# Optimization experiments

Measured on AMD Instinct MI355X. Metric: run time of the kernel, lower is better.

Reference implementation:

```python
import jax, jax.numpy as jnp
import numpy as np

B, T, L, A, O = 16, 32, 64, 64, 16
EL, EA, EO = 128, 128, 128
FL, FA, FO, C = 256, 256, 256, 768


def setup_inputs() -> dict:
    key = jax.random.key(0)
    ks = jax.random.split(key, 16)
    s = 0.02
    return {
        "lab_feats": jax.random.normal(ks[0], (B, T, L, FL), jnp.float32),
        "abn_feats": jax.random.normal(ks[1], (B, T, A, FA), jnp.float32),
        "lab_concept_emb": jax.random.normal(ks[2], (L, C), jnp.float32),
        "abn_concept_emb": jax.random.normal(ks[3], (A, C), jnp.float32),
        "lab_rel_emb": jax.random.normal(ks[4], (EL, C), jnp.float32),
        "abn_rel_emb": jax.random.normal(ks[5], (EA, C), jnp.float32),
        "W_lab": jax.random.normal(ks[6], (FL + C, FL), jnp.float32) * s,
        "b_lab": jnp.zeros((FL,), jnp.float32),
        "W_abn": jax.random.normal(ks[7], (FA + C, FA), jnp.float32) * s,
        "b_abn": jnp.zeros((FA,), jnp.float32),
        "W_org": jax.random.normal(ks[8], (FL, FO), jnp.float32) * s,
        "b_org": jnp.zeros((FO,), jnp.float32),
        "D": jax.random.normal(ks[9], (C, FL), jnp.float32) * s,
        "W_o2a": jax.random.normal(ks[10], (FO, FA), jnp.float32) * s,
        "b_o2a": jnp.zeros((FA,), jnp.float32),
        "time_mask": jnp.ones((B, T), dtype=bool),
        "lab_idx": jax.random.randint(ks[11], (EL,), 0, L),
        "lab_org_idx": jax.random.randint(ks[12], (EL,), 0, O),
        "abn_idx": jax.random.randint(ks[13], (EA,), 0, A),
        "abn_org_idx": jax.random.randint(ks[14], (EA,), 0, O),
        "o2a_abn_idx": jax.random.randint(ks[15], (EO,), 0, A),
        "o2a_org_idx": jax.random.randint(jax.random.fold_in(key, 99), (EO,), 0, O),
        "num_organs": O,
    }


def _scatter_mean(attended, org_idx, num_organs, time_mask):
    # attended: (B,T,E,F); emulate legacy per-edge accumulate: cnt[o] = deg(o)*w(b,t)
    onehot = (org_idx[:, None] == jnp.arange(num_organs)[None, :]).astype(attended.dtype)  # (E,O)
    sum_o = jnp.einsum('btef,eo->btof', attended, onehot)
    deg = onehot.sum(0)                                    # (O,)
    w = time_mask.astype(attended.dtype)                   # (B,T)
    cnt = w[:, :, None] * deg[None, None, :]               # (B,T,O)
    mean_o = sum_o / jnp.maximum(cnt, 1e-9)[..., None]
    return mean_o, cnt > 0


def reference(lab_feats, abn_feats, lab_concept_emb, abn_concept_emb,
              lab_rel_emb, abn_rel_emb, W_lab, b_lab, W_abn, b_abn,
              W_org, b_org, D, W_o2a, b_o2a,
              time_mask, lab_idx, lab_org_idx, abn_idx, abn_org_idx,
              o2a_abn_idx, o2a_org_idx, num_organs):
    Fl = lab_feats.shape[-1]
    Fa = abn_feats.shape[-1]
    A_ = abn_feats.shape[2]

    # --- lab -> organ: gather, concat(feat, concept+relation), W_lab (split to avoid concat) ---
    x = lab_feats[:, :, lab_idx, :]                        # (B,T,El,Fl)
    c = lab_concept_emb[lab_idx] + lab_rel_emb             # (El,C)
    h = jnp.tanh(jnp.einsum('btef,fg->bteg', x, W_lab[:Fl]) + c @ W_lab[Fl:] + b_lab)
    attended = h + lab_rel_emb @ D                         # relation-projection D
    mean_lab, mask_lab = _scatter_mean(attended, lab_org_idx, num_organs, time_mask)

    # --- abn -> organ ---
    xa = abn_feats[:, :, abn_idx, :]
    ca = abn_concept_emb[abn_idx] + abn_rel_emb
    ha = jnp.tanh(jnp.einsum('btef,fg->bteg', xa, W_abn[:Fa]) + ca @ W_abn[Fa:] + b_abn)
    mean_abn, mask_abn = _scatter_mean(ha, abn_org_idx, num_organs, time_mask)

    # --- organ states ---
    organ_states = jnp.tanh(jnp.einsum('btof,fg->btog', mean_lab + mean_abn, W_org) + b_org)
    organ_states = organ_states * (mask_lab | mask_abn)[..., None].astype(organ_states.dtype)

    # --- organ -> abnormality message passing (mean over incident organs) ---
    msg = jnp.einsum('btog,gf->btof', organ_states, W_o2a) + b_o2a   # (B,T,O,Fa)
    gathered = msg[:, :, o2a_org_idx, :]                   # (B,T,Eo,Fa)
    onehot = (o2a_abn_idx[:, None] == jnp.arange(A_)[None, :]).astype(msg.dtype)  # (Eo,A)
    agg = jnp.einsum('btef,ea->btaf', gathered, onehot)
    deg = jnp.maximum(onehot.sum(0), 1.0)                  # (A,)
    abn_out = abn_feats + agg / deg[None, None, :, None]
    return abn_out
```

## Files before the change

### kernel.cpp

```cpp
#include <hip/hip_runtime.h>
#include <math.h>

#define NBT 512
#define NF  256
#define NC  768
#define NROW 64
#define NORG 16
#define NE  128
#define SLD 260
#define SY  264
#define SSR 776

#define WS_SW_LAB1 0
#define WS_SW_ABN1 131072
#define WS_SW_ORG  1441792
#define WS_SW_O2A  1572864
#define WS_LAB_CB  1753088
#define WS_ABN_CB  1884160
#define WS_ADDSUM  2015232
#define WS_WCNT    2031616
#define WS_INVL    2035712
#define WS_INVA    2035776
#define WS_MASK    2035840
#define WS_SRTL    2035904
#define WS_SRTA    2036544
#define WS_NEED    2097152

typedef __attribute__((ext_vector_type(8)))  short bf16x8;
typedef __attribute__((ext_vector_type(16))) float f32x16;
typedef __attribute__((ext_vector_type(4)))  float f32x4;

__device__ __forceinline__ short f2bf(float f) {
    union { float f; unsigned u; } v; v.f = f;
    unsigned r = v.u + 0x7FFF + ((v.u >> 16) & 1);
    return (short)(r >> 16);
}
__device__ __forceinline__ float bf2f(short s) {
    return __uint_as_float(((unsigned)(unsigned short)s) << 16);
}
__device__ __forceinline__ float tanh_fast(float x) {
    float xc = fminf(fmaxf(x, -15.f), 15.f);
    float e = __expf(2.f * xc);
    return 1.f - 2.f * __builtin_amdgcn_rcpf(e + 1.f);
}
__device__ __forceinline__ f32x16 mfma32(bf16x8 a, bf16x8 b, f32x16 c) {
    return __builtin_amdgcn_mfma_f32_32x32x16_bf16(a, b, c, 0, 0, 0);
}
__device__ __forceinline__ f32x4 mfma16(bf16x8 a, bf16x8 b, f32x4 c) {
    return __builtin_amdgcn_mfma_f32_16x16x32_bf16(a, b, c, 0, 0, 0);
}
__device__ __forceinline__ bf16x8 pack_a16(const float* __restrict__ p) {
    float4 x0 = *(const float4*)p;
    float4 x1 = *(const float4*)(p + 4);
    union { bf16x8 v; unsigned u[4]; } r;
    r.u[0] = __builtin_amdgcn_perm(__float_as_uint(x0.y), __float_as_uint(x0.x), 0x07060302);
    r.u[1] = __builtin_amdgcn_perm(__float_as_uint(x0.w), __float_as_uint(x0.z), 0x07060302);
    r.u[2] = __builtin_amdgcn_perm(__float_as_uint(x1.y), __float_as_uint(x1.x), 0x07060302);
    r.u[3] = __builtin_amdgcn_perm(__float_as_uint(x1.w), __float_as_uint(x1.z), 0x07060302);
    return r.v;
}

__device__ __forceinline__ void swz32(const float* __restrict__ src, short* __restrict__ dst, int s) {
    const int l = s & 63, rest = s >> 6;
    const int nt = rest & 7, k16 = rest >> 3;
    const int n = nt * 32 + (l & 31);
    const int kb = k16 * 16 + ((l >> 5) & 1) * 8;
    bf16x8 v;
    #pragma unroll
    for (int j = 0; j < 8; ++j) v[j] = f2bf(src[(kb + j) * NF + n]);
    *(bf16x8*)(dst + s * 8) = v;
}
__device__ __forceinline__ void swz16(const float* __restrict__ src, short* __restrict__ dst, int s) {
    const int l = s & 63, rest = s >> 6;
    const int nt = rest & 15, k32 = rest >> 4;
    const int n = nt * 16 + (l & 15);
    const int kb = k32 * 32 + ((l >> 4) & 3) * 8;
    bf16x8 v;
    #pragma unroll
    for (int j = 0; j < 8; ++j) v[j] = f2bf(src[(kb + j) * NF + n]);
    *(bf16x8*)(dst + s * 8) = v;
}

__global__ __launch_bounds__(256) void pk_pre2(
    const float* __restrict__ W_lab, const float* __restrict__ W_abn,
    const float* __restrict__ W_org,
    const float* __restrict__ W_o2a, const float* __restrict__ D,
    const float* __restrict__ lab_rel,
    const float* __restrict__ lab_con, const float* __restrict__ abn_con,
    const float* __restrict__ abn_rel,
    const float* __restrict__ b_lab, const float* __restrict__ b_abn,
    const int* __restrict__ lab_idx, const int* __restrict__ lab_org_idx,
    const int* __restrict__ abn_idx, const int* __restrict__ abn_org_idx,
    const int* __restrict__ o2a_abn_idx, const int* __restrict__ o2a_org_idx,
    char* __restrict__ ws) {
    __shared__ __align__(16) float sP[4 * 1024];
    __shared__ __align__(16) short sSR[NORG * SSR];
    const int bid = blockIdx.x;
    const int tid = threadIdx.x;
    if (bid < 8) {
        #pragma unroll
        for (int c = 0; c < 3; ++c) {
            const int k = c * 256 + tid;
            float s[16];
            #pragma unroll
            for (int o = 0; o < 16; ++o) s[o] = 0.f;
            #pragma unroll 8
            for (int e = 0; e < NE; ++e) {
                const float v = lab_rel[e * NC + k];
                const int o = lab_org_idx[e];
                #pragma unroll
                for (int oo = 0; oo < 16; ++oo) s[oo] += (o == oo) ? v : 0.f;
            }
            #pragma unroll
            for (int o = 0; o < 16; ++o) sSR[o * SSR + k] = f2bf(s[o]);
        }
        __syncthreads();
        const int nb = bid;
        const int l = tid & 63, w = tid >> 6;
        f32x16 acc;
        #pragma unroll
        for (int r = 0; r < 16; ++r) acc[r] = 0.f;
        const int row = l & 31;
        const int kk = ((l >> 5) & 1) * 8;
        const int n = nb * 32 + (l & 31);
        #pragma unroll 4
        for (int k16 = 0; k16 < 12; ++k16) {
            const int k = w * 192 + k16 * 16 + kk;
            bf16x8 af;
            if (row < NORG) {
                af = *(const bf16x8*)(sSR + row * SSR + k);
            } else {
                #pragma unroll
                for (int j = 0; j < 8; ++j) af[j] = 0;
            }
            const float* dp = D + k * NF + n;
            bf16x8 bv;
            #pragma unroll
            for (int j = 0; j < 8; ++j) bv[j] = f2bf(dp[j * NF]);
            acc = mfma32(af, bv, acc);
        }
        #pragma unroll
        for (int r = 0; r < 16; ++r) sP[w * 1024 + r * 64 + l] = acc[r];
        __syncthreads();
        float* outp = (float*)(ws + WS_ADDSUM);
        #pragma unroll
        for (int q = 0; q < 4; ++q) {
            const int idx2 = q * 256 + tid;
            float v = sP[idx2] + sP[1024 + idx2] + sP[2048 + idx2] + sP[3072 + idx2];
            const int reg = idx2 >> 6, ll = idx2 & 63;
            const int er = (reg & 3) + 8 * (reg >> 2) + 4 * (ll >> 5);
            const int col = nb * 32 + (ll & 31);
            if (er < NORG) outp[er * NF + col] = v;
        }
    } else if (bid < 72) {
        const int l = tid & 63, w = tid >> 6;
        const int b = bid - 8;
        const int side = b >> 5;
        const int b2 = b & 31;
        const int mq = b2 >> 3, nb = b2 & 7;
        const int em = mq * 32;
        const float* W2  = side ? (W_abn + NF * NF) : (W_lab + NF * NF);
        const float* con = side ? abn_con : lab_con;
        const float* rel = side ? abn_rel : lab_rel;
        const int*   idx = side ? abn_idx : lab_idx;

        f32x16 acc;
        #pragma unroll
        for (int r = 0; r < 16; ++r) acc[r] = 0.f;

        const int e  = em + (l & 31);
        const int kk = ((l >> 5) & 1) * 8;
        const int n  = nb * 32 + (l & 31);
        const float* cp = con + idx[e] * NC;
        const float* rp = rel + e * NC;
        #pragma unroll 4
        for (int k16 = 0; k16 < 12; ++k16) {
            const int k = (w * 12 + k16) * 16 + kk;
            float4 c0 = *(const float4*)(cp + k);
            float4 c1 = *(const float4*)(cp + k + 4);
            float4 r0 = *(const float4*)(rp + k);
            float4 r1 = *(const float4*)(rp + k + 4);
            float v[8] = {c0.x + r0.x, c0.y + r0.y, c0.z + r0.z, c0.w + r0.w,
                          c1.x + r1.x, c1.y + r1.y, c1.z + r1.z, c1.w + r1.w};
            bf16x8 af;
            #pragma unroll
            for (int j = 0; j < 8; ++j) af[j] = f2bf(v[j]);
            const float* wp = W2 + k * NF + n;
            bf16x8 bv;
            #pragma unroll
            for (int j = 0; j < 8; ++j) bv[j] = f2bf(wp[j * NF]);
            acc = mfma32(af, bv, acc);
        }
        #pragma unroll
        for (int r = 0; r < 16; ++r) sP[w * 1024 + r * 64 + l] = acc[r];
        __syncthreads();
        float* outp = (float*)(ws + (side ? WS_ABN_CB : WS_LAB_CB));
        const float* bias = side ? b_abn : b_lab;
        #pragma unroll
        for (int q = 0; q < 4; ++q) {
            const int idx2 = q * 256 + tid;
            float v = sP[idx2] + sP[1024 + idx2] + sP[2048 + idx2] + sP[3072 + idx2];
            const int reg = idx2 >> 6, ll = idx2 & 63;
            const int er = (reg & 3) + 8 * (reg >> 2) + 4 * (ll >> 5);
            const int col = nb * 32 + (ll & 31);
            outp[(em + er) * NF + col] = v + bias[col];
        }
    } else if (bid == 72) {
        __shared__ int cL[NORG], cA[NORG], cC[NROW * NORG];
        __shared__ int goL[NORG + 1], goA[NORG + 1], curL[NORG], curA[NORG];
        const int t = tid;
        for (int i = t; i < NROW * NORG; i += 256) cC[i] = 0;
        if (t < NORG) { cL[t] = 0; cA[t] = 0; }
        __syncthreads();
        if (t < NE) {
            atomicAdd(&cL[lab_org_idx[t]], 1);
            atomicAdd(&cA[abn_org_idx[t]], 1);
            atomicAdd(&cC[o2a_abn_idx[t] * NORG + o2a_org_idx[t]], 1);
        }
        __syncthreads();
        if (t == 0) { int s = 0; for (int o = 0; o < NORG; ++o) { goL[o] = s; s += cL[o]; } goL[NORG] = s; }
        if (t == 1) { int s = 0; for (int o = 0; o < NORG; ++o) { goA[o] = s; s += cA[o]; } goA[NORG] = s; }
        __syncthreads();
        if (t < NORG) { curL[t] = goL[t]; curA[t] = goA[t]; }
        __syncthreads();
        if (t < NE) {
            const int ol = lab_org_idx[t], oa = abn_org_idx[t];
            int p = atomicAdd(&curL[ol], 1);
            ((int*)(ws + WS_SRTL))[p] = (lab_idx[t] << 24) | (ol << 16) | t;
            int q = atomicAdd(&curA[oa], 1);
            ((int*)(ws + WS_SRTA))[q] = (abn_idx[t] << 24) | (oa << 16) | t;
        }
        if (t < NORG) {
            ((float*)(ws + WS_INVL))[t] = cL[t] ? 1.f / (float)cL[t] : 0.f;
            ((float*)(ws + WS_INVA))[t] = cA[t] ? 1.f / (float)cA[t] : 0.f;
            ((float*)(ws + WS_MASK))[t] = (cL[t] || cA[t]) ? 1.f : 0.f;
        }
        if (t < NROW) {
            int dega = 0;
            for (int o = 0; o < NORG; ++o) dega += cC[t * NORG + o];
            float inv = 1.f / (float)(dega > 1 ? dega : 1);
            for (int o = 0; o < NORG; ++o)
                ((float*)(ws + WS_WCNT))[t * NORG + o] = (float)cC[t * NORG + o] * inv;
        }
    } else {
        const int gid = (bid - 73) * 256 + tid;
        if      (gid <  8192) swz32(W_lab, (short*)(ws + WS_SW_LAB1), gid);
        else if (gid < 16384) swz32(W_abn, (short*)(ws + WS_SW_ABN1), gid - 8192);
        else if (gid < 24576) swz16(W_org, (short*)(ws + WS_SW_ORG),  gid - 16384);
        else                  swz16(W_o2a, (short*)(ws + WS_SW_O2A),  gid - 24576);
    }
}

template <int POST>
__device__ __forceinline__ void gemm_small8(
    const float* __restrict__ sIn, const short* __restrict__ Bsw,
    const float* __restrict__ bias, const float* __restrict__ mask,
    float* __restrict__ sOut, int tid) {
    const int l = tid & 63, w = tid >> 6;
    f32x4 acc[2];
    #pragma unroll
    for (int i = 0; i < 2; ++i) { acc[i][0] = 0.f; acc[i][1] = 0.f; acc[i][2] = 0.f; acc[i][3] = 0.f; }
    #pragma unroll 2
    for (int k32 = 0; k32 < 8; ++k32) {
        const float* ap = sIn + (l & 15) * SLD + k32 * 32 + ((l >> 4) & 3) * 8;
        bf16x8 af = pack_a16(ap);
        #pragma unroll
        for (int nt = 0; nt < 2; ++nt) {
            bf16x8 bfv = *(const bf16x8*)(Bsw + ((k32 * 16 + w * 2 + nt) * 64 + l) * 8);
            acc[nt] = mfma16(af, bfv, acc[nt]);
        }
    }
    #pragma unroll
    for (int nt = 0; nt < 2; ++nt) {
        const int col = (w * 2 + nt) * 16 + (l & 15);
        const float b = bias[col];
        #pragma unroll
        for (int reg = 0; reg < 4; ++reg) {
            const int row = ((l >> 4) & 3) * 4 + reg;
            float v = acc[nt][reg] + b;
            if (POST == 0) v = tanh_fast(v) * mask[row];
            sOut[row * SLD + col] = v;
        }
    }
}

__global__ __launch_bounds__(512, 2) void kg_fuse2(
    const float* __restrict__ lab_feats, const float* __restrict__ abn_feats,
    const float* __restrict__ b_org, const float* __restrict__ b_o2a,
    const char* __restrict__ ws, float* __restrict__ out) {
    __shared__ __align__(16) short sY[NROW * SY];
    __shared__ __align__(16) float sAcc[NORG * SLD];
    __shared__ float sWc[NROW * NORG];
    __shared__ int sEL[NE], sEA[NE];
    __shared__ float sOv[2 * NF];
    __shared__ float sInvL[NORG], sInvA[NORG], sMsk[NORG];

    const int tid = threadIdx.x;
    const int bt = blockIdx.x;

    if (tid < NE)          sEL[tid]      = ((const int*)(ws + WS_SRTL))[tid];
    else if (tid < 2 * NE) sEA[tid - NE] = ((const int*)(ws + WS_SRTA))[tid - NE];
    else {
        const int u = tid - 2 * NE;
        if      (u < 16) sInvL[u]       = ((const float*)(ws + WS_INVL))[u];
        else if (u < 32) sInvA[u - 16]  = ((const float*)(ws + WS_INVA))[u - 16];
        else if (u < 48) sMsk[u - 32]   = ((const float*)(ws + WS_MASK))[u - 32];
    }
    #pragma unroll
    for (int i = tid; i < NROW * NORG; i += 512)
        sWc[i] = ((const float*)(ws + WS_WCNT))[i];
    #pragma unroll
    for (int i = tid; i < NORG * NF; i += 512)
        sAcc[(i >> 8) * SLD + (i & 255)] = 0.f;

    const float* addR = (const float*)(ws + WS_ADDSUM);
    const int l = tid & 63, w = tid >> 6;

    for (int side = 0; side < 2; ++side) {
        const float* X   = (side ? abn_feats : lab_feats) + bt * (NROW * NF);
        const short* Bsw = (const short*)(ws + (side ? WS_SW_ABN1 : WS_SW_LAB1));
        const float* cb  = (const float*)(ws + (side ? WS_ABN_CB : WS_LAB_CB));
        const int* sE    = side ? sEA : sEL;

        __syncthreads();
        #pragma unroll
        for (int ss = 0; ss < 4; ++ss) {
            const int s = tid + 512 * ss;
            const int k16 = s >> 7, rt = (s >> 6) & 1, ll = s & 63;
            const int row = rt * 32 + (ll & 31);
            const int kb = k16 * 16 + ((ll >> 5) & 1) * 8;
            *(bf16x8*)(sY + s * 8) = pack_a16(X + row * NF + kb);
        }
        __syncthreads();
        f32x16 acc[2];
        #pragma unroll
        for (int i = 0; i < 2; ++i)
            #pragma unroll
            for (int r = 0; r < 16; ++r) acc[i][r] = 0.f;
        #pragma unroll 8
        for (int k16 = 0; k16 < 16; ++k16) {
            bf16x8 a0 = *(const bf16x8*)(sY + ((k16 * 2 + 0) * 64 + l) * 8);
            bf16x8 a1 = *(const bf16x8*)(sY + ((k16 * 2 + 1) * 64 + l) * 8);
            bf16x8 b0 = *(const bf16x8*)(Bsw + ((k16 * 8 + w) * 64 + l) * 8);
            acc[0] = mfma32(a0, b0, acc[0]);
            acc[1] = mfma32(a1, b0, acc[1]);
        }
        __syncthreads();
        {
            const int col = w * 32 + (l & 31);
            #pragma unroll
            for (int rt = 0; rt < 2; ++rt)
                #pragma unroll
                for (int reg = 0; reg < 16; ++reg) {
                    const int row = rt * 32 + (reg & 3) + 8 * (reg >> 2) + 4 * (l >> 5);
                    sY[row * SY + col] = f2bf(acc[rt][reg]);
                }
        }
        __syncthreads();

        const int eh = tid >> 8;
        const int t = tid & 255;
        const short* yt = sY + t;
        const float* cbt = cb + t;
        const int ob0 = (__builtin_amdgcn_readfirstlane(sE[63]) >> 16) & 255;
        const int ob1 = (__builtin_amdgcn_readfirstlane(sE[64]) >> 16) & 255;
        const bool bshared = (ob0 == ob1);
        const int ebase = eh * 64;
        float racc = 0.f;
        int curo = (__builtin_amdgcn_readfirstlane(sE[ebase]) >> 16) & 255;
        for (int i0 = 0; i0 < 64; i0 += 8) {
            int   pk8[8];
            float cb8[8], y8[8];
            #pragma unroll
            for (int j = 0; j < 8; ++j) {
                const int pk = __builtin_amdgcn_readfirstlane(sE[ebase + i0 + j]);
                pk8[j] = pk;
                cb8[j] = cbt[(pk & 0xffff) * NF];
                y8[j]  = bf2f(yt[(pk >> 24) * SY]);
            }
            #pragma unroll
            for (int j = 0; j < 8; ++j) {
                const int o = (pk8[j] >> 16) & 255;
                if (o != curo) {
                    if (bshared && curo == ob0) sOv[eh * NF + t] = racc;
                    else if (side == 0) sAcc[curo * SLD + t] = (racc + addR[curo * NF + t]) * sInvL[curo];
                    else                sAcc[curo * SLD + t] += racc * sInvA[curo];
                    racc = 0.f; curo = o;
                }
                racc += tanh_fast(y8[j] + cb8[j]);
            }
        }
        if (bshared && curo == ob0) sOv[eh * NF + t] = racc;
        else if (side == 0) sAcc[curo * SLD + t] = (racc + addR[curo * NF + t]) * sInvL[curo];
        else                sAcc[curo * SLD + t] += racc * sInvA[curo];

        if (bshared) {
            __syncthreads();
            if (tid < NF) {
                const float v = sOv[tid] + sOv[NF + tid];
                if (side == 0) sAcc[ob0 * SLD + tid] = (v + addR[ob0 * NF + tid]) * sInvL[ob0];
                else           sAcc[ob0 * SLD + tid] += v * sInvA[ob0];
            }
        }
    }
    __syncthreads();

    float* sSt  = (float*)sY;
    float* sMsg = (float*)sY + NORG * SLD;
    gemm_small8<0>(sAcc, (const short*)(ws + WS_SW_ORG), b_org, sMsk, sSt, tid);
    __syncthreads();
    gemm_small8<1>(sSt, (const short*)(ws + WS_SW_O2A), b_o2a, nullptr, sMsg, tid);
    __syncthreads();

    {
        const int t = tid & 255, rh = tid >> 8;
        float mr[NORG];
        #pragma unroll
        for (int o = 0; o < NORG; ++o) mr[o] = sMsg[o * SLD + t];
        const float* src = abn_feats + bt * (NROW * NF);
        float* dst = out + bt * (NROW * NF);
        #pragma unroll 8
        for (int a0 = 0; a0 < 32; ++a0) {
            const int a = rh * 32 + a0;
            float s = src[a * NF + t];
            #pragma unroll
            for (int o = 0; o < NORG; ++o) s += sWc[a * NORG + o] * mr[o];
            dst[a * NF + t] = s;
        }
    }
}

__device__ __forceinline__ void stage_A(const float* __restrict__ X, short* __restrict__ sA, int tid) {
    #pragma unroll
    for (int ss = 0; ss < 8; ++ss) {
        const int s = tid + 256 * ss;
        const int k16 = s >> 7, rt = (s >> 6) & 1, l = s & 63;
        const int row = rt * 32 + (l & 31);
        const int kb = k16 * 16 + ((l >> 5) & 1) * 8;
        *(bf16x8*)(sA + s * 8) = pack_a16(X + row * NF + kb);
    }
}

template <int POST>
__device__ __forceinline__ void gemm_small(
    const float* __restrict__ sIn, const short* __restrict__ Bsw,
    const float* __restrict__ bias, const float* __restrict__ mask,
    float* __restrict__ sOut, int tid) {
    const int l = tid & 63, w = tid >> 6;
    f32x4 acc[4];
    #pragma unroll
    for (int i = 0; i < 4; ++i) { acc[i][0] = 0.f; acc[i][1] = 0.f; acc[i][2] = 0.f; acc[i][3] = 0.f; }
    #pragma unroll 2
    for (int k32 = 0; k32 < 8; ++k32) {
        const float* ap = sIn + (l & 15) * SLD + k32 * 32 + ((l >> 4) & 3) * 8;
        bf16x8 af = pack_a16(ap);
        #pragma unroll
        for (int nt = 0; nt < 4; ++nt) {
            bf16x8 bfv = *(const bf16x8*)(Bsw + ((k32 * 16 + w * 4 + nt) * 64 + l) * 8);
            acc[nt] = mfma16(af, bfv, acc[nt]);
        }
    }
    #pragma unroll
    for (int nt = 0; nt < 4; ++nt) {
        const int col = w * 64 + nt * 16 + (l & 15);
        const float b = bias[col];
        #pragma unroll
        for (int reg = 0; reg < 4; ++reg) {
            const int row = ((l >> 4) & 3) * 4 + reg;
            float v = acc[nt][reg] + b;
            if (POST == 0) v = tanh_fast(v) * mask[row];
            sOut[row * SLD + col] = v;
        }
    }
}

template <bool LAB>
__device__ __forceinline__ void side_pass(
    const float* __restrict__ X, const short* __restrict__ Bsw,
    const float* __restrict__ cb, const float* __restrict__ addR,
    const float* __restrict__ sInv, const int* __restrict__ sE,
    short* __restrict__ sA, float* __restrict__ sAcc, int tid) {
    __syncthreads();
    stage_A(X, sA, tid);
    __syncthreads();
    const int l = tid & 63, w = tid >> 6;
    f32x16 acc[2][2];
    #pragma unroll
    for (int i = 0; i < 2; ++i)
        #pragma unroll
        for (int j = 0; j < 2; ++j)
            #pragma unroll
            for (int r = 0; r < 16; ++r) acc[i][j][r] = 0.f;
    #pragma unroll 8
    for (int k16 = 0; k16 < 16; ++k16) {
        bf16x8 a0 = *(const bf16x8*)(sA + ((k16 * 2 + 0) * 64 + l) * 8);
        bf16x8 a1 = *(const bf16x8*)(sA + ((k16 * 2 + 1) * 64 + l) * 8);
        bf16x8 b0 = *(const bf16x8*)(Bsw + ((k16 * 8 + 2 * w + 0) * 64 + l) * 8);
        bf16x8 b1 = *(const bf16x8*)(Bsw + ((k16 * 8 + 2 * w + 1) * 64 + l) * 8);
        acc[0][0] = mfma32(a0, b0, acc[0][0]);
        acc[1][0] = mfma32(a1, b0, acc[1][0]);
        acc[0][1] = mfma32(a0, b1, acc[0][1]);
        acc[1][1] = mfma32(a1, b1, acc[1][1]);
    }
    __syncthreads();
    short* sYs = sA;
    #pragma unroll
    for (int rt = 0; rt < 2; ++rt)
        #pragma unroll
        for (int nt = 0; nt < 2; ++nt) {
            const int col = w * 64 + nt * 32 + (l & 31);
            #pragma unroll
            for (int reg = 0; reg < 16; ++reg) {
                const int row = rt * 32 + (reg & 3) + 8 * (reg >> 2) + 4 * (l >> 5);
                sYs[row * SY + col] = f2bf(acc[rt][nt][reg]);
            }
        }
    __syncthreads();
    const int t = tid;
    if (LAB) {
        #pragma unroll
        for (int o = 0; o < NORG; ++o)
            sAcc[o * SLD + t] = addR[o * NF + t] * sInv[o];
    }
    float racc = 0.f;
    int curo = (sE[0] >> 16) & 255;
    #pragma unroll 4
    for (int i = 0; i < NE; ++i) {
        const int pk = sE[i];
        const int o = (pk >> 16) & 255;
        if (o != curo) {
            sAcc[curo * SLD + t] += racc * sInv[curo];
            racc = 0.f; curo = o;
        }
        const float yv = bf2f(sYs[(pk >> 24) * SY + t]);
        racc += tanh_fast(yv + cb[(pk & 0xffff) * NF + t]);
    }
    sAcc[curo * SLD + t] += racc * sInv[curo];
}

__global__ __launch_bounds__(256, 2) void kg_main(
    const float* __restrict__ lab_feats, const float* __restrict__ abn_feats,
    const float* __restrict__ b_org, const float* __restrict__ b_o2a,
    const char* __restrict__ ws, float* __restrict__ out) {
    __shared__ __align__(16) short sY[NROW * SY];
    __shared__ __align__(16) float sAcc[NORG * SLD];
    __shared__ __align__(16) float sSt [NORG * SLD];
    __shared__ int   sEL[NE], sEA[NE];
    __shared__ float sInvL[NORG], sInvA[NORG], sMsk[NORG];

    const int tid = threadIdx.x;
    const int bt = blockIdx.x;

    if (tid < NE) {
        sEL[tid] = ((const int*)(ws + WS_SRTL))[tid];
        sEA[tid] = ((const int*)(ws + WS_SRTA))[tid];
    } else {
        const int u = tid - NE;
        if      (u < 16) sInvL[u]      = ((const float*)(ws + WS_INVL))[u];
        else if (u < 32) sInvA[u - 16] = ((const float*)(ws + WS_INVA))[u - 16];
        else if (u < 48) sMsk[u - 32]  = ((const float*)(ws + WS_MASK))[u - 32];
    }

    const float* Xl = lab_feats + bt * (NROW * NF);
    const float* Xa = abn_feats + bt * (NROW * NF);
    side_pass<true >(Xl, (const short*)(ws + WS_SW_LAB1),
                     (const float*)(ws + WS_LAB_CB), (const float*)(ws + WS_ADDSUM),
                     sInvL, sEL, sY, sAcc, tid);
    side_pass<false>(Xa, (const short*)(ws + WS_SW_ABN1),
                     (const float*)(ws + WS_ABN_CB), nullptr,
                     sInvA, sEA, sY, sAcc, tid);
    __syncthreads();

    gemm_small<0>(sAcc, (const short*)(ws + WS_SW_ORG), b_org, sMsk, sSt, tid);
    __syncthreads();
    float* sMsg = sAcc;
    gemm_small<1>(sSt, (const short*)(ws + WS_SW_O2A), b_o2a, nullptr, sMsg, tid);
    __syncthreads();

    {
        const int g = tid;
        float mr[NORG];
        #pragma unroll
        for (int o = 0; o < NORG; ++o) mr[o] = sMsg[o * SLD + g];
        const float* src = abn_feats + bt * (NROW * NF);
        float* dst = out + bt * (NROW * NF);
        const float* wc = (const float*)(ws + WS_WCNT);
        #pragma unroll 4
        for (int a = 0; a < NROW; ++a) {
            float s = src[a * NF + g];
            #pragma unroll
            for (int o = 0; o < NORG; ++o) s += wc[a * NORG + o] * mr[o];
            dst[a * NF + g] = s;
        }
    }
}

extern "C" void kernel_launch(void* const* d_in, const int* in_sizes, int n_in,
                              void* d_out, int out_size, void* d_ws, size_t ws_size,
                              hipStream_t stream) {
    const float* lab_feats   = (const float*)d_in[0];
    const float* abn_feats   = (const float*)d_in[1];
    const float* lab_concept = (const float*)d_in[2];
    const float* abn_concept = (const float*)d_in[3];
    const float* lab_rel     = (const float*)d_in[4];
    const float* abn_rel     = (const float*)d_in[5];
    const float* W_lab       = (const float*)d_in[6];
    const float* b_lab       = (const float*)d_in[7];
    const float* W_abn       = (const float*)d_in[8];
    const float* b_abn       = (const float*)d_in[9];
    const float* W_org       = (const float*)d_in[10];
    const float* b_org       = (const float*)d_in[11];
    const float* D           = (const float*)d_in[12];
    const float* W_o2a       = (const float*)d_in[13];
    const float* b_o2a       = (const float*)d_in[14];
    const int* lab_idx     = (const int*)d_in[16];
    const int* lab_org_idx = (const int*)d_in[17];
    const int* abn_idx     = (const int*)d_in[18];
    const int* abn_org_idx = (const int*)d_in[19];
    const int* o2a_abn_idx = (const int*)d_in[20];
    const int* o2a_org_idx = (const int*)d_in[21];
    char* ws = (char*)d_ws;
    float* out = (float*)d_out;

    pk_pre2<<<201, 256, 0, stream>>>(W_lab, W_abn, W_org, W_o2a, D, lab_rel,
                                     lab_concept, abn_concept, abn_rel,
                                     b_lab, b_abn,
                                     lab_idx, lab_org_idx, abn_idx, abn_org_idx,
                                     o2a_abn_idx, o2a_org_idx, ws);
    if (ws_size >= (size_t)WS_NEED) {
        kg_fuse2<<<NBT, 512, 0, stream>>>(lab_feats, abn_feats, b_org, b_o2a, ws, out);
    } else {
        kg_main<<<NBT, 256, 0, stream>>>(lab_feats, abn_feats, b_org, b_o2a, ws, out);
    }
}
```

Measured before the change: 234.0 us.

## Fold relation-projection term into a precomputed per-organ bias for organ GEMM

The per-organ constant contribution from the summed relation embeddings times D is pushed through W_org ahead of time (D@W_org, then scaled by inverse degree) into a per-organ bias matrix. The main kernel then skips adding the addsum term and uses a row-dependent bias in the organ GEMM. The serial 8-block relation-sum pass in the preprocess kernel is also split across 48 parallel blocks. This adds an extra small launch (pk_mid) and a larger workspace, but shortens the critical preprocess path and removes some per-element work from the fused kernel.

Measured after the change: 198.9 us. 15.0% less time.

```diff
diff --git a/kernel.cpp b/kernel.cpp
--- a/kernel.cpp
+++ b/kernel.cpp
@@ -9,14 +9,15 @@
 #define NE  128
 #define SLD 260
 #define SY  264
-#define SSR 776
 
 #define WS_SW_LAB1 0
 #define WS_SW_ABN1 131072
 #define WS_SW_ORG  1441792
 #define WS_SW_O2A  1572864
+#define WS_SUMREL  1703936
 #define WS_LAB_CB  1753088
 #define WS_ABN_CB  1884160
+#define WS_BORG    2015232
 #define WS_ADDSUM  2015232
 #define WS_WCNT    2031616
 #define WS_INVL    2035712
@@ -24,7 +25,8 @@
 #define WS_MASK    2035840
 #define WS_SRTL    2035904
 #define WS_SRTA    2036544
-#define WS_NEED    2097152
+#define WS_DW      2097152
+#define WS_NEED    2883584
 
 typedef __attribute__((ext_vector_type(8)))  short bf16x8;
 typedef __attribute__((ext_vector_type(16))) float f32x16;
@@ -94,69 +96,12 @@
     const int* __restrict__ o2a_abn_idx, const int* __restrict__ o2a_org_idx,
     char* __restrict__ ws) {
     __shared__ __align__(16) float sP[4 * 1024];
-    __shared__ __align__(16) short sSR[NORG * SSR];
     const int bid = blockIdx.x;
     const int tid = threadIdx.x;
-    if (bid < 8) {
-        #pragma unroll
-        for (int c = 0; c < 3; ++c) {
-            const int k = c * 256 + tid;
-            float s[16];
-            #pragma unroll
-            for (int o = 0; o < 16; ++o) s[o] = 0.f;
-            #pragma unroll 8
-            for (int e = 0; e < NE; ++e) {
-                const float v = lab_rel[e * NC + k];
-                const int o = lab_org_idx[e];
-                #pragma unroll
-                for (int oo = 0; oo < 16; ++oo) s[oo] += (o == oo) ? v : 0.f;
-            }
-            #pragma unroll
-            for (int o = 0; o < 16; ++o) sSR[o * SSR + k] = f2bf(s[o]);
-        }
-        __syncthreads();
-        const int nb = bid;
+    if (bid < 64) {
         const int l = tid & 63, w = tid >> 6;
-        f32x16 acc;
-        #pragma unroll
-        for (int r = 0; r < 16; ++r) acc[r] = 0.f;
-        const int row = l & 31;
-        const int kk = ((l >> 5) & 1) * 8;
-        const int n = nb * 32 + (l & 31);
-        #pragma unroll 4
-        for (int k16 = 0; k16 < 12; ++k16) {
-            const int k = w * 192 + k16 * 16 + kk;
-            bf16x8 af;
-            if (row < NORG) {
-                af = *(const bf16x8*)(sSR + row * SSR + k);
-            } else {
-                #pragma unroll
-                for (int j = 0; j < 8; ++j) af[j] = 0;
-            }
-            const float* dp = D + k * NF + n;
-            bf16x8 bv;
-            #pragma unroll
-            for (int j = 0; j < 8; ++j) bv[j] = f2bf(dp[j * NF]);
-            acc = mfma32(af, bv, acc);
-        }
-        #pragma unroll
-        for (int r = 0; r < 16; ++r) sP[w * 1024 + r * 64 + l] = acc[r];
-        __syncthreads();
-        float* outp = (float*)(ws + WS_ADDSUM);
-        #pragma unroll
-        for (int q = 0; q < 4; ++q) {
-            const int idx2 = q * 256 + tid;
-            float v = sP[idx2] + sP[1024 + idx2] + sP[2048 + idx2] + sP[3072 + idx2];
-            const int reg = idx2 >> 6, ll = idx2 & 63;
-            const int er = (reg & 3) + 8 * (reg >> 2) + 4 * (ll >> 5);
-            const int col = nb * 32 + (ll & 31);
-            if (er < NORG) outp[er * NF + col] = v;
-        }
-    } else if (bid < 72) {
-        const int l = tid & 63, w = tid >> 6;
-        const int b = bid - 8;
-        const int side = b >> 5;
-        const int b2 = b & 31;
+        const int side = bid >> 5;
+        const int b2 = bid & 31;
         const int mq = b2 >> 3, nb = b2 & 7;
         const int em = mq * 32;
         const float* W2  = side ? (W_abn + NF * NF) : (W_lab + NF * NF);
@@ -205,7 +150,18 @@
             const int col = nb * 32 + (ll & 31);
             outp[(em + er) * NF + col] = v + bias[col];
         }
-    } else if (bid == 72) {
+    } else if (bid < 112) {
+        const int b2 = bid - 64;
+        const int o = b2 / 3, kth = b2 % 3;
+        const int k = kth * 256 + tid;
+        float s = 0.f;
+        #pragma unroll 16
+        for (int e = 0; e < NE; ++e) {
+            const float v = lab_rel[e * NC + k];
+            s += (lab_org_idx[e] == o) ? v : 0.f;
+        }
+        ((float*)(ws + WS_SUMREL))[o * NC + k] = s;
+    } else if (bid == 112) {
         __shared__ int cL[NORG], cA[NORG], cC[NROW * NORG];
         __shared__ int goL[NORG + 1], goA[NORG + 1], curL[NORG], curA[NORG];
         const int t = tid;
@@ -242,19 +198,104 @@
             for (int o = 0; o < NORG; ++o)
                 ((float*)(ws + WS_WCNT))[t * NORG + o] = (float)cC[t * NORG + o] * inv;
         }
-    } else {
-        const int gid = (bid - 73) * 256 + tid;
+    } else if (bid < 241) {
+        const int gid = (bid - 113) * 256 + tid;
         if      (gid <  8192) swz32(W_lab, (short*)(ws + WS_SW_LAB1), gid);
         else if (gid < 16384) swz32(W_abn, (short*)(ws + WS_SW_ABN1), gid - 8192);
         else if (gid < 24576) swz16(W_org, (short*)(ws + WS_SW_ORG),  gid - 16384);
         else                  swz16(W_o2a, (short*)(ws + WS_SW_O2A),  gid - 24576);
-    }
-}
-
-template <int POST>
-__device__ __forceinline__ void gemm_small8(
+    } else {
+        const int b = bid - 241;
+        const int mq = b >> 3, nb = b & 7;
+        const int l = tid & 63, w = tid >> 6;
+        f32x16 acc;
+        #pragma unroll
+        for (int r = 0; r < 16; ++r) acc[r] = 0.f;
+        const int row = mq * 32 + (l & 31);
+        const int kk = ((l >> 5) & 1) * 8;
+        const int n = nb * 32 + (l & 31);
+        #pragma unroll
+        for (int k16 = 0; k16 < 4; ++k16) {
+            const int k = w * 64 + k16 * 16 + kk;
+            bf16x8 af = pack_a16(D + row * NF + k);
+            const float* wp = W_org + k * NF + n;
+            bf16x8 bv;
+            #pragma unroll
+            for (int j = 0; j < 8; ++j) bv[j] = f2bf(wp[j * NF]);
+            acc = mfma32(af, bv, acc);
+        }
+        #pragma unroll
+        for (int r = 0; r < 16; ++r) sP[w * 1024 + r * 64 + l] = acc[r];
+        __syncthreads();
+        float* outp = (float*)(ws + WS_DW);
+        #pragma unroll
+        for (int q = 0; q < 4; ++q) {
+            const int idx2 = q * 256 + tid;
+            float v = sP[idx2] + sP[1024 + idx2] + sP[2048 + idx2] + sP[3072 + idx2];
+            const int reg = idx2 >> 6, ll = idx2 & 63;
+            const int er = (reg & 3) + 8 * (reg >> 2) + 4 * (ll >> 5);
+            const int col = nb * 32 + (ll & 31);
+            outp[(mq * 32 + er) * NF + col] = v;
+        }
+    }
+}
+
+__global__ __launch_bounds__(256) void pk_mid(
+    const float* __restrict__ b_org, char* __restrict__ ws) {
+    __shared__ __align__(16) float sP[4 * 1024];
+    const int tid = threadIdx.x;
+    const int nb = blockIdx.x;
+    const int l = tid & 63, w = tid >> 6;
+    const float* sr = (const float*)(ws + WS_SUMREL);
+    const float* dw = (const float*)(ws + WS_DW);
+    const float* invL = (const float*)(ws + WS_INVL);
+    f32x16 acc;
+    #pragma unroll
+    for (int r = 0; r < 16; ++r) acc[r] = 0.f;
+    const int row = l & 31;
+    const int kk = ((l >> 5) & 1) * 8;
+    const int n = nb * 32 + (l & 31);
+    const float il = (row < NORG) ? invL[row] : 0.f;
+    const float* cp = sr + row * NC;
+    #pragma unroll 4
+    for (int k16 = 0; k16 < 12; ++k16) {
+        const int k = w * 192 + k16 * 16 + kk;
+        bf16x8 af;
+        if (row < NORG) {
+            float4 x0 = *(const float4*)(cp + k);
+            float4 x1 = *(const float4*)(cp + k + 4);
+            af[0] = f2bf(x0.x * il); af[1] = f2bf(x0.y * il);
+            af[2] = f2bf(x0.z * il); af[3] = f2bf(x0.w * il);
+            af[4] = f2bf(x1.x * il); af[5] = f2bf(x1.y * il);
+            af[6] = f2bf(x1.z * il); af[7] = f2bf(x1.w * il);
+        } else {
+            #pragma unroll
+            for (int j = 0; j < 8; ++j) af[j] = 0;
+        }
+        const float* dp = dw + k * NF + n;
+        bf16x8 bv;
+        #pragma unroll
+        for (int j = 0; j < 8; ++j) bv[j] = f2bf(dp[j * NF]);
+        acc = mfma32(af, bv, acc);
+    }
+    #pragma unroll
+    for (int r = 0; r < 16; ++r) sP[w * 1024 + r * 64 + l] = acc[r];
+    __syncthreads();
+    float* outp = (float*)(ws + WS_BORG);
+    #pragma unroll
+    for (int q = 0; q < 4; ++q) {
+        const int idx2 = q * 256 + tid;
+        float v = sP[idx2] + sP[1024 + idx2] + sP[2048 + idx2] + sP[3072 + idx2];
+        const int reg = idx2 >> 6, ll = idx2 & 63;
+        const int er = (reg & 3) + 8 * (reg >> 2) + 4 * (ll >> 5);
+        const int col = nb * 32 + (ll & 31);
+        if (er < NORG) outp[er * NF + col] = v + b_org[col];
+    }
+}
+
+__device__ __forceinline__ void gemm_small8_borg(
     const float* __restrict__ sIn, const short* __restrict__ Bsw,
-    const float* __restrict__ bias, const float* __restrict__ mask,
+    const float* __restrict__ borg, const float* __restrict__ mask,
     float* __restrict__ sOut, int tid) {
     const int l = tid & 63, w = tid >> 6;
     f32x4 acc[2];
@@ -273,20 +314,46 @@
     #pragma unroll
     for (int nt = 0; nt < 2; ++nt) {
         const int col = (w * 2 + nt) * 16 + (l & 15);
-        const float b = bias[col];
         #pragma unroll
         for (int reg = 0; reg < 4; ++reg) {
             const int row = ((l >> 4) & 3) * 4 + reg;
-            float v = acc[nt][reg] + b;
-            if (POST == 0) v = tanh_fast(v) * mask[row];
-            sOut[row * SLD + col] = v;
+            float v = acc[nt][reg] + borg[row * NF + col];
+            sOut[row * SLD + col] = tanh_fast(v) * mask[row];
+        }
+    }
+}
+__device__ __forceinline__ void gemm_small8_vec(
+    const float* __restrict__ sIn, const short* __restrict__ Bsw,
+    const float* __restrict__ bias, float* __restrict__ sOut, int tid) {
+    const int l = tid & 63, w = tid >> 6;
+    f32x4 acc[2];
+    #pragma unroll
+    for (int i = 0; i < 2; ++i) { acc[i][0] = 0.f; acc[i][1] = 0.f; acc[i][2] = 0.f; acc[i][3] = 0.f; }
+    #pragma unroll 2
+    for (int k32 = 0; k32 < 8; ++k32) {
+        const float* ap = sIn + (l & 15) * SLD + k32 * 32 + ((l >> 4) & 3) * 8;
+        bf16x8 af = pack_a16(ap);
+        #pragma unroll
+        for (int nt = 0; nt < 2; ++nt) {
+            bf16x8 bfv = *(const bf16x8*)(Bsw + ((k32 * 16 + w * 2 + nt) * 64 + l) * 8);
+            acc[nt] = mfma16(af, bfv, acc[nt]);
+        }
+    }
+    #pragma unroll
+    for (int nt = 0; nt < 2; ++nt) {
+        const int col = (w * 2 + nt) * 16 + (l & 15);
+        const float b = bias[col];
+        #pragma unroll
+        for (int reg = 0; reg < 4; ++reg) {
+            const int row = ((l >> 4) & 3) * 4 + reg;
+            sOut[row * SLD + col] = acc[nt][reg] + b;
         }
     }
 }
 
 __global__ __launch_bounds__(512, 2) void kg_fuse2(
     const float* __restrict__ lab_feats, const float* __restrict__ abn_feats,
-    const float* __restrict__ b_org, const float* __restrict__ b_o2a,
+    const float* __restrict__ b_o2a,
     const char* __restrict__ ws, float* __restrict__ out) {
     __shared__ __align__(16) short sY[NROW * SY];
     __shared__ __align__(16) float sAcc[NORG * SLD];
@@ -313,7 +380,6 @@
     for (int i = tid; i < NORG * NF; i += 512)
         sAcc[(i >> 8) * SLD + (i & 255)] = 0.f;
 
-    const float* addR = (const float*)(ws + WS_ADDSUM);
     const int l = tid & 63, w = tid >> 6;
 
     for (int side = 0; side < 2; ++side) {
@@ -321,6 +387,7 @@
         const short* Bsw = (const short*)(ws + (side ? WS_SW_ABN1 : WS_SW_LAB1));
         const float* cb  = (const float*)(ws + (side ? WS_ABN_CB : WS_LAB_CB));
         const int* sE    = side ? sEA : sEL;
+        const float* sInv = side ? sInvA : sInvL;
 
         __syncthreads();
         #pragma unroll
@@ -383,22 +450,22 @@
                 const int o = (pk8[j] >> 16) & 255;
                 if (o != curo) {
                     if (bshared && curo == ob0) sOv[eh * NF + t] = racc;
-                    else if (side == 0) sAcc[curo * SLD + t] = (racc + addR[curo * NF + t]) * sInvL[curo];
-                    else                sAcc[curo * SLD + t] += racc * sInvA[curo];
+                    else if (side == 0) sAcc[curo * SLD + t] = racc * sInv[curo];
+                    else                sAcc[curo * SLD + t] += racc * sInv[curo];
                     racc = 0.f; curo = o;
                 }
                 racc += tanh_fast(y8[j] + cb8[j]);
             }
         }
         if (bshared && curo == ob0) sOv[eh * NF + t] = racc;
-        else if (side == 0) sAcc[curo * SLD + t] = (racc + addR[curo * NF + t]) * sInvL[curo];
-        else                sAcc[curo * SLD + t] += racc * sInvA[curo];
+        else if (side == 0) sAcc[curo * SLD + t] = racc * sInv[curo];
+        else                sAcc[curo * SLD + t] += racc * sInv[curo];
 
         if (bshared) {
             __syncthreads();
             if (tid < NF) {
                 const float v = sOv[tid] + sOv[NF + tid];
-                if (side == 0) sAcc[ob0 * SLD + tid] = (v + addR[ob0 * NF + tid]) * sInvL[ob0];
+                if (side == 0) sAcc[ob0 * SLD + tid] = v * sInvL[ob0];
                 else           sAcc[ob0 * SLD + tid] += v * sInvA[ob0];
             }
         }
@@ -407,9 +474,10 @@
 
     float* sSt  = (float*)sY;
     float* sMsg = (float*)sY + NORG * SLD;
-    gemm_small8<0>(sAcc, (const short*)(ws + WS_SW_ORG), b_org, sMsk, sSt, tid);
-    __syncthreads();
-    gemm_small8<1>(sSt, (const short*)(ws + WS_SW_O2A), b_o2a, nullptr, sMsg, tid);
+    gemm_small8_borg(sAcc, (const short*)(ws + WS_SW_ORG),
+                     (const float*)(ws + WS_BORG), sMsk, sSt, tid);
+    __syncthreads();
+    gemm_small8_vec(sSt, (const short*)(ws + WS_SW_O2A), b_o2a, sMsg, tid);
     __syncthreads();
 
     {
@@ -427,6 +495,51 @@
             for (int o = 0; o < NORG; ++o) s += sWc[a * NORG + o] * mr[o];
             dst[a * NF + t] = s;
         }
+    }
+}
+
+__global__ __launch_bounds__(256) void pk_addsum_fb(const float* __restrict__ D,
+                                                    char* __restrict__ ws) {
+    __shared__ __align__(16) float sP[4 * 1024];
+    const int tid = threadIdx.x;
+    const int nb = blockIdx.x;
+    const int l = tid & 63, w = tid >> 6;
+    const float* sr = (const float*)(ws + WS_SUMREL);
+    f32x16 acc;
+    #pragma unroll
+    for (int r = 0; r < 16; ++r) acc[r] = 0.f;
+    const int row = l & 31;
+    const int kk = ((l >> 5) & 1) * 8;
+    const int n = nb * 32 + (l & 31);
+    const float* cp = sr + row * NC;
+    #pragma unroll 4
+    for (int k16 = 0; k16 < 12; ++k16) {
+        const int k = w * 192 + k16 * 16 + kk;
+        bf16x8 af;
+        if (row < NORG) {
+            af = pack_a16(cp + k);
+        } else {
+            #pragma unroll
+            for (int j = 0; j < 8; ++j) af[j] = 0;
+        }
+        const float* dp = D + k * NF + n;
+        bf16x8 bv;
+        #pragma unroll
+        for (int j = 0; j < 8; ++j) bv[j] = f2bf(dp[j * NF]);
+        acc = mfma32(af, bv, acc);
+    }
+    #pragma unroll
+    for (int r = 0; r < 16; ++r) sP[w * 1024 + r * 64 + l] = acc[r];
+    __syncthreads();
+    float* outp = (float*)(ws + WS_ADDSUM);
+    #pragma unroll
+    for (int q = 0; q < 4; ++q) {
+        const int idx2 = q * 256 + tid;
+        float v = sP[idx2] + sP[1024 + idx2] + sP[2048 + idx2] + sP[3072 + idx2];
+        const int reg = idx2 >> 6, ll = idx2 & 63;
+        const int er = (reg & 3) + 8 * (reg >> 2) + 4 * (ll >> 5);
+        const int col = nb * 32 + (ll & 31);
+        if (er < NORG) outp[er * NF + col] = v;
     }
 }
 
@@ -622,14 +735,21 @@
     char* ws = (char*)d_ws;
     float* out = (float*)d_out;
 
-    pk_pre2<<<201, 256, 0, stream>>>(W_lab, W_abn, W_org, W_o2a, D, lab_rel,
-                                     lab_concept, abn_concept, abn_rel,
-                                     b_lab, b_abn,
-                                     lab_idx, lab_org_idx, abn_idx, abn_org_idx,
-                                     o2a_abn_idx, o2a_org_idx, ws);
     if (ws_size >= (size_t)WS_NEED) {
-        kg_fuse2<<<NBT, 512, 0, stream>>>(lab_feats, abn_feats, b_org, b_o2a, ws, out);
+        pk_pre2<<<433, 256, 0, stream>>>(W_lab, W_abn, W_org, W_o2a, D, lab_rel,
+                                         lab_concept, abn_concept, abn_rel,
+                                         b_lab, b_abn,
+                                         lab_idx, lab_org_idx, abn_idx, abn_org_idx,
+                                         o2a_abn_idx, o2a_org_idx, ws);
+        pk_mid<<<8, 256, 0, stream>>>(b_org, ws);
+        kg_fuse2<<<NBT, 512, 0, stream>>>(lab_feats, abn_feats, b_o2a, ws, out);
     } else {
+        pk_pre2<<<241, 256, 0, stream>>>(W_lab, W_abn, W_org, W_o2a, D, lab_rel,
+                                         lab_concept, abn_concept, abn_rel,
+                                         b_lab, b_abn,
+                                         lab_idx, lab_org_idx, abn_idx, abn_org_idx,
+                                         o2a_abn_idx, o2a_org_idx, ws);
+        pk_addsum_fb<<<8, 256, 0, stream>>>(D, ws);
         kg_main<<<NBT, 256, 0, stream>>>(lab_feats, abn_feats, b_org, b_o2a, ws, out);
     }
 }
```
